# Performance work log

Hardware: AMD Instinct MI355X
Metric: run time of the kernel (lower is better)

Reference implementation:

```python
import jax, jax.numpy as jnp
import numpy as np

D_MODEL = 768
N_HEADS = 4
N_POINTS = 4
PATCH = 16
IMG = 224
HF = IMG // PATCH  # 14
WF = IMG // PATCH  # 14
LQ = HF * WF       # 196 tokens
DH = D_MODEL // N_HEADS  # 192


def setup_inputs() -> dict:
    key = jax.random.key(0)
    ks = jax.random.split(key, 14)
    s = 0.02
    inp = {
        "x": jax.random.normal(ks[0], (4, 16, 3, IMG, IMG), dtype=jnp.float32),
        # patch-embed conv (Conv2d 3->768, k=16, s=16)
        "embed_w": s * jax.random.normal(ks[1], (D_MODEL, 3, PATCH, PATCH), dtype=jnp.float32),
        "embed_b": jnp.zeros((D_MODEL,), dtype=jnp.float32),
        # MSDeformAttn linears (nn.Linear stores W as [out, in]; y = x @ W.T + b)
        "value_w": s * jax.random.normal(ks[2], (D_MODEL, D_MODEL), dtype=jnp.float32),
        "value_b": jnp.zeros((D_MODEL,), dtype=jnp.float32),
        "off_w": s * jax.random.normal(ks[3], (N_HEADS * N_POINTS * 2, D_MODEL), dtype=jnp.float32),
        "off_b": s * jax.random.normal(ks[4], (N_HEADS * N_POINTS * 2,), dtype=jnp.float32),
        "aw_w": s * jax.random.normal(ks[5], (N_HEADS * N_POINTS, D_MODEL), dtype=jnp.float32),
        "aw_b": jnp.zeros((N_HEADS * N_POINTS,), dtype=jnp.float32),
        "outp_w": s * jax.random.normal(ks[6], (D_MODEL, D_MODEL), dtype=jnp.float32),
        "outp_b": jnp.zeros((D_MODEL,), dtype=jnp.float32),
        # final nn.Linear proj
        "proj_w": s * jax.random.normal(ks[7], (D_MODEL, D_MODEL), dtype=jnp.float32),
        "proj_b": jnp.zeros((D_MODEL,), dtype=jnp.float32),
    }
    return inp


def _patch_embed(x, w, b):
    # x: (N,3,H,W); non-overlapping 16x16 patches == Conv2d(3,D,16,16)
    N = x.shape[0]
    xh = x.reshape(N, 3, HF, PATCH, WF, PATCH)
    feat = jnp.einsum('nchpwq,dcpq->nhwd', xh, w) + b  # (N,HF,WF,D)
    return feat.reshape(N, LQ, D_MODEL)


def _ref_points():
    lin = jnp.linspace(0.0, 1.0, HF)
    gy, gx = jnp.meshgrid(lin, lin, indexing='ij')
    return jnp.stack([gx, gy], -1).reshape(LQ, 2)  # (Lq, 2) in [0,1], (x,y)


def _deform_attn_core(value, loc, attn):
    # value: (N, Lq, M, Dh); loc: (N, Lq, M, P, 2) normalized [0,1]; attn: (N, Lq, M, P)
    N = value.shape[0]
    # grid_sample align_corners=False: pixel = (2*loc-1 + 1)*S/2 - 0.5 = loc*S - 0.5
    px = loc[..., 0] * WF - 0.5
    py = loc[..., 1] * HF - 0.5
    x0 = jnp.floor(px).astype(jnp.int32)
    y0 = jnp.floor(py).astype(jnp.int32)
    x1, y1 = x0 + 1, y0 + 1
    wx1 = px - x0.astype(px.dtype)
    wy1 = py - y0.astype(py.dtype)
    wx0, wy0 = 1.0 - wx1, 1.0 - wy1

    valh = value.transpose(0, 2, 1, 3)  # (N, M, HW, Dh)

    def gather(ix, iy):
        valid = (ix >= 0) & (ix < WF) & (iy >= 0) & (iy < HF)  # zeros padding
        idx = jnp.clip(iy, 0, HF - 1) * WF + jnp.clip(ix, 0, WF - 1)
        idxm = idx.transpose(0, 2, 1, 3).reshape(N, N_HEADS, LQ * N_POINTS)
        g = jnp.take_along_axis(valh, idxm[..., None], axis=2)  # (N,M,Lq*P,Dh)
        g = g * valid.transpose(0, 2, 1, 3).reshape(N, N_HEADS, LQ * N_POINTS, 1)
        return g.reshape(N, N_HEADS, LQ, N_POINTS, DH)

    def w4(a, b):  # (N,Lq,M,P) -> (N,M,Lq,P,1)
        return (a * b).transpose(0, 2, 1, 3)[..., None]

    sampled = (w4(wx0, wy0) * gather(x0, y0) + w4(wx1, wy0) * gather(x1, y0)
               + w4(wx0, wy1) * gather(x0, y1) + w4(wx1, wy1) * gather(x1, y1))
    # weighted combine over points
    out = (sampled * attn.transpose(0, 2, 1, 3)[..., None]).sum(3)  # (N,M,Lq,Dh)
    return out.transpose(0, 2, 1, 3).reshape(N, LQ, D_MODEL)


def reference(x, embed_w, embed_b, value_w, value_b, off_w, off_b, aw_w, aw_b,
              outp_w, outp_b, proj_w, proj_b):
    B, T = x.shape[0], x.shape[1]
    N = B * T
    xi = x.reshape(N, 3, IMG, IMG)
    feat = _patch_embed(xi, embed_w, embed_b)  # (N, Lq, D)

    # MSDeformAttn (n_levels=1)
    value = (feat @ value_w.T + value_b).reshape(N, LQ, N_HEADS, DH)
    off = (feat @ off_w.T + off_b).reshape(N, LQ, N_HEADS, N_POINTS, 2)
    aw = (feat @ aw_w.T + aw_b).reshape(N, LQ, N_HEADS, N_POINTS)
    aw = jax.nn.softmax(aw, axis=-1)  # softmax over n_levels*n_points = 4

    ref = _ref_points()  # (Lq, 2)
    norm = jnp.array([WF, HF], dtype=feat.dtype)  # offset_normalizer = (W, H)
    loc = ref[None, :, None, None, :] + off / norm  # (N,Lq,M,P,2)

    out = _deform_attn_core(value, loc, aw)
    out = out @ outp_w.T + outp_b  # output_proj

    pooled = out.mean(axis=1)  # mean over tokens
    final = pooled @ proj_w.T + proj_b
    return final.reshape(B, T, D_MODEL)
```

## Files before the change

### kernel.cpp

```cpp
#include <hip/hip_runtime.h>
#include <hip/hip_bf16.h>


using bf16 = __bf16;
typedef bf16  bf16x4 __attribute__((ext_vector_type(4)));
typedef bf16  bf16x8 __attribute__((ext_vector_type(8)));
typedef float f32x4  __attribute__((ext_vector_type(4)));

#define N_IMG   64
#define LQ      196
#define DM      768
#define NH      4
#define DH      192
#define M_ROWS  (N_IMG * LQ)
#define NCAT    896

#define P_WET    0
#define P_WCAT   288
#define P_BCAT   624
#define P_ZERO   628
#define PREP_GRID 676

#define B_WGEMM   0
#define B_IM2COL  42
#define STAGE_GRID (B_IM2COL + 9408)

#define OFF_A     ((size_t)0)
#define OFF_WC    (OFF_A     + 19267584)
#define OFF_BCAT  (OFF_WC    + 1376256)
#define OFF_VBUF  (OFF_BCAT  + 4096)
#define OFF_OA    (OFF_VBUF  + 19267584)
#define OFF_CORE  (OFF_OA    + 3211264)
#define OFF_POOL  (OFF_CORE  + 196608)
#define OFF_WCATB (OFF_POOL  + 196608)
#define OFF_WET   (OFF_WCATB + 1376256)

__device__ __forceinline__ void gload_lds16(const bf16* g, bf16* l) {
#if __has_builtin(__builtin_amdgcn_global_load_lds)
  __builtin_amdgcn_global_load_lds(
      (const __attribute__((address_space(1))) void*)g,
      (__attribute__((address_space(3))) void*)l, 16, 0, 0);
#else
  *(bf16x8*)l = *(const bf16x8*)g;
#endif
}

__global__ void prep_kernel(const float* __restrict__ embed_w,
                            const float* __restrict__ embed_b,
                            const float* __restrict__ value_w,
                            const float* __restrict__ off_w,
                            const float* __restrict__ aw_w,
                            const float* __restrict__ value_b,
                            const float* __restrict__ off_b,
                            const float* __restrict__ aw_b,
                            bf16* __restrict__ WeT,
                            bf16* __restrict__ Wcatb,
                            float* __restrict__ bcat2,
                            float* __restrict__ core) {
  const int bid = blockIdx.x;
  const int tid = threadIdx.x;

  if (bid < P_WCAT) {
    const int t = bid * 256 + tid;
    const int e = t / 96;
    const int g = t - e * 96;
    bf16x8 o;
#pragma unroll
    for (int j = 0; j < 8; ++j)
      o[j] = (bf16)embed_w[(size_t)(g * 8 + j) * DM + e];
    *(bf16x8*)(WeT + (size_t)e * DM + g * 8) = o;
    return;
  }

  if (bid < P_BCAT) {
    const int t = (bid - P_WCAT) * 256 + tid;
    const int rr = t / 96;
    const int g  = t - rr * 96;
    const float* src = (rr < 768) ? value_w + (size_t)rr * DM
                     : (rr < 800) ? off_w + (size_t)(rr - 768) * DM
                     : (rr < 816) ? aw_w + (size_t)(rr - 800) * DM : nullptr;
    bf16x8 o;
    if (src) {
      const float4 f0 = *(const float4*)(src + g * 8);
      const float4 f1 = *(const float4*)(src + g * 8 + 4);
      o[0] = (bf16)f0.x; o[1] = (bf16)f0.y; o[2] = (bf16)f0.z; o[3] = (bf16)f0.w;
      o[4] = (bf16)f1.x; o[5] = (bf16)f1.y; o[6] = (bf16)f1.z; o[7] = (bf16)f1.w;
    } else {
#pragma unroll
      for (int j = 0; j < 8; ++j) o[j] = (bf16)0.f;
    }
    *(bf16x8*)(Wcatb + (size_t)rr * DM + g * 8) = o;
    return;
  }

  if (bid < P_ZERO) {
    const int o = (bid - P_BCAT) * 256 + tid;
    if (o < NCAT) {
      float bias_o = (o < 768) ? value_b[o]
                   : (o < 800) ? off_b[o - 768]
                   : (o < 816) ? aw_b[o - 800] : 0.f;
      float acc = 0.f;
      if (o < 816) {
        const float* wr = (o < 768) ? value_w + (size_t)o * DM
                        : (o < 800) ? off_w + (size_t)(o - 768) * DM
                        : aw_w + (size_t)(o - 800) * DM;
        const float4* w4p = (const float4*)wr;
        const float4* b4p = (const float4*)embed_b;
#pragma unroll 4
        for (int k = 0; k < DM / 4; ++k) {
          const float4 wv = w4p[k], bv = b4p[k];
          acc += wv.x * bv.x + wv.y * bv.y + wv.z * bv.z + wv.w * bv.w;
        }
      }
      bcat2[o] = acc + bias_o;
    }
    return;
  }

  const int i = (bid - P_ZERO) * 256 + tid;
  f32x4 z = {0.f, 0.f, 0.f, 0.f};
  ((f32x4*)core)[i] = z;
}

__global__ void stage_kernel(const float* __restrict__ x,
                             const bf16* __restrict__ Wcatb,
                             const bf16* __restrict__ WeT,
                             bf16* __restrict__ A,
                             bf16* __restrict__ Wc) {
  const int bid = blockIdx.x;
  const int tid = threadIdx.x;

  if (bid >= B_IM2COL) {
    const int t   = (bid - B_IM2COL) * 256 + tid;
    const int row = t / 192;
    const int j   = t - row * 192;
    const int k   = j * 4;
    const int c   = k >> 8;
    const int r   = k & 255;
    const int p   = r >> 4;
    const int q   = r & 15;
    const int n   = row / 196;
    const int lq  = row - n * 196;
    const int h   = lq / 14;
    const int w   = lq - h * 14;
    const float4 v = *(const float4*)(x +
        ((((size_t)n * 3 + c) * 224) + h * 16 + p) * 224 + w * 16 + q);
    bf16x4 o;
    o[0] = (bf16)v.x; o[1] = (bf16)v.y; o[2] = (bf16)v.z; o[3] = (bf16)v.w;
    *(bf16x4*)(A + (size_t)row * DM + k) = o;
    return;
  }

  const int mT = bid / 6;
  const int nT = bid - mT * 6;
  const int oBase = mT * 128;
  const int eBase = nT * 128;
  const int wave = tid >> 6;
  const int lane = tid & 63;
  const int quad = lane >> 4;
  const int r16  = lane & 15;
  const int wm = wave & 1;
  const int wn = wave >> 1;

  const f32x4 zero = {0.f, 0.f, 0.f, 0.f};
  f32x4 acc[4][4];
#pragma unroll
  for (int mi = 0; mi < 4; ++mi)
#pragma unroll
    for (int ni = 0; ni < 4; ++ni) acc[mi][ni] = zero;

  const bf16* Ab = Wcatb + (size_t)(oBase + wm * 64 + r16) * DM + quad * 8;
  const bf16* Bb = WeT   + (size_t)(eBase + wn * 64 + r16) * DM + quad * 8;

#pragma unroll 2
  for (int kk = 0; kk < DM; kk += 32) {
    bf16x8 af[4], bfr[4];
#pragma unroll
    for (int mi = 0; mi < 4; ++mi)
      af[mi] = *(const bf16x8*)(Ab + (size_t)mi * 16 * DM + kk);
#pragma unroll
    for (int ni = 0; ni < 4; ++ni)
      bfr[ni] = *(const bf16x8*)(Bb + (size_t)ni * 16 * DM + kk);
#pragma unroll
    for (int mi = 0; mi < 4; ++mi)
#pragma unroll
      for (int ni = 0; ni < 4; ++ni)
        acc[mi][ni] = __builtin_amdgcn_mfma_f32_16x16x32_bf16(
            af[mi], bfr[ni], acc[mi][ni], 0, 0, 0);
  }

#pragma unroll
  for (int ni = 0; ni < 4; ++ni) {
    const int col = eBase + wn * 64 + ni * 16 + r16;
#pragma unroll
    for (int mi = 0; mi < 4; ++mi) {
      const int row0 = oBase + wm * 64 + mi * 16 + quad * 4;
#pragma unroll
      for (int rr = 0; rr < 4; ++rr)
        Wc[(size_t)(row0 + rr) * DM + col] = (bf16)acc[mi][ni][rr];
    }
  }
}

__global__ void gemm2_mixed(const bf16* __restrict__ A, const bf16* __restrict__ B,
                            const float* __restrict__ bias,
                            bf16* __restrict__ Vb, float* __restrict__ OA,
                            int M, int N, int K) {
  __shared__ bf16 As[128 * 64];
  __shared__ bf16 Bs[128 * 64];

  const int tid  = threadIdx.x;
  const int wave = tid >> 6;
  const int lane = tid & 63;
  const int nBase = blockIdx.x * 128;
  const int mBase = blockIdx.y * 128;
  const int wm = wave & 1;
  const int wn = wave >> 1;
  const int quad = lane >> 4;
  const int r16  = lane & 15;

  const f32x4 zero = {0.f, 0.f, 0.f, 0.f};
  f32x4 acc[4][4];
#pragma unroll
  for (int mi = 0; mi < 4; ++mi)
#pragma unroll
    for (int ni = 0; ni < 4; ++ni) acc[mi][ni] = zero;

  const int srow = wave * 32 + (lane >> 3);
  const int scol = (lane & 7) * 8;
  const bf16* Ag = A + (size_t)(mBase + srow) * K + scol;
  const bf16* Bg = B + (size_t)(nBase + srow) * K + scol;
  bf16* Al = As + srow * 64 + scol;
  bf16* Bl = Bs + srow * 64 + scol;

  for (int kt = 0; kt < K; kt += 64) {
#pragma unroll
    for (int i = 0; i < 4; ++i) {
      gload_lds16(Ag + (size_t)(i * 8) * K + kt, Al + i * 8 * 64);
      gload_lds16(Bg + (size_t)(i * 8) * K + kt, Bl + i * 8 * 64);
    }
    __syncthreads();
#pragma unroll
    for (int kk = 0; kk < 64; kk += 32) {
      bf16x8 af[4], bfr[4];
#pragma unroll
      for (int mi = 0; mi < 4; ++mi)
        af[mi] = *(const bf16x8*)&As[(wm * 64 + mi * 16 + r16) * 64 + kk + quad * 8];
#pragma unroll
      for (int ni = 0; ni < 4; ++ni)
        bfr[ni] = *(const bf16x8*)&Bs[(wn * 64 + ni * 16 + r16) * 64 + kk + quad * 8];
#pragma unroll
      for (int mi = 0; mi < 4; ++mi)
#pragma unroll
        for (int ni = 0; ni < 4; ++ni)
          acc[mi][ni] = __builtin_amdgcn_mfma_f32_16x16x32_bf16(
              af[mi], bfr[ni], acc[mi][ni], 0, 0, 0);
    }
    __syncthreads();
  }

#pragma unroll
  for (int ni = 0; ni < 4; ++ni) {
    const int col = nBase + wn * 64 + ni * 16 + r16;
    const float bv = bias[col];
#pragma unroll
    for (int mi = 0; mi < 4; ++mi) {
      const int row0 = mBase + wm * 64 + mi * 16 + quad * 4;
#pragma unroll
      for (int rr = 0; rr < 4; ++rr) {
        float v = acc[mi][ni][rr] + bv;
        int row = row0 + rr;
        if (col < 768) {
          Vb[(size_t)row * 768 + col] = (bf16)v;
        } else if (col < 816) {
          OA[(size_t)row * 64 + (col - 768)] = v;
        }
      }
    }
  }
}

__global__ void deform_kernel(const bf16* __restrict__ Vb,
                              const float* __restrict__ OA,
                              float* __restrict__ core) {
  __shared__ float s_w[64][4];
  __shared__ int   s_t[64][4];

  const int n   = blockIdx.x;
  const int lq0 = blockIdx.y * 4;
  const int z   = blockIdx.z;
  const int tid = threadIdx.x;

  if (tid < 64) {
    const int i = tid >> 4;
    const int m = (tid >> 2) & 3;
    const int p = tid & 3;
    const int lq = lq0 + i;
    const float* row = OA + ((size_t)n * LQ + lq) * 64;

    const float l0 = row[32 + m * 4 + 0];
    const float l1 = row[32 + m * 4 + 1];
    const float l2 = row[32 + m * 4 + 2];
    const float l3 = row[32 + m * 4 + 3];
    const float mx = fmaxf(fmaxf(l0, l1), fmaxf(l2, l3));
    const float e0 = __expf(l0 - mx), e1 = __expf(l1 - mx);
    const float e2 = __expf(l2 - mx), e3 = __expf(l3 - mx);
    const float inv = 1.f / (e0 + e1 + e2 + e3);
    const float ep[4] = {e0, e1, e2, e3};
    const float ew = ep[p] * inv;

    const int h = lq / 14, w = lq - (lq / 14) * 14;
    const float px = (float)w * (14.f / 13.f) - 0.5f + row[(m * 4 + p) * 2 + 0];
    const float py = (float)h * (14.f / 13.f) - 0.5f + row[(m * 4 + p) * 2 + 1];
    const float fx = floorf(px), fy = floorf(py);
    const int x0 = (int)fx, y0 = (int)fy;
    const float wx1 = px - fx, wy1 = py - fy;
    const float wx0 = 1.f - wx1, wy0 = 1.f - wy1;

    const bool vx0 = (x0 >= 0) & (x0 < 14);
    const bool vx1 = (x0 >= -1) & (x0 < 13);
    const bool vy0 = (y0 >= 0) & (y0 < 14);
    const bool vy1 = (y0 >= -1) & (y0 < 13);
    const int cx0 = min(max(x0, 0), 13),      cx1 = min(max(x0 + 1, 0), 13);
    const int cy0 = min(max(y0, 0), 13) * 14, cy1 = min(max(y0 + 1, 0), 13) * 14;

    s_w[tid][0] = (vx0 & vy0) ? ew * wx0 * wy0 : 0.f;
    s_w[tid][1] = (vx1 & vy0) ? ew * wx1 * wy0 : 0.f;
    s_w[tid][2] = (vx0 & vy1) ? ew * wx0 * wy1 : 0.f;
    s_w[tid][3] = (vx1 & vy1) ? ew * wx1 * wy1 : 0.f;
    s_t[tid][0] = cy0 + cx0;
    s_t[tid][1] = cy0 + cx1;
    s_t[tid][2] = cy1 + cx0;
    s_t[tid][3] = cy1 + cx1;
  }
  __syncthreads();

  const int ch = z * 256 + tid;
  const int m  = ch / DH;
  const bf16* vb = Vb + (size_t)n * LQ * 768 + ch;
  float acc = 0.f;
#pragma unroll
  for (int i = 0; i < 4; ++i) {
#pragma unroll
    for (int p = 0; p < 4; ++p) {
      const int e = i * 16 + m * 4 + p;
      const float4 w4 = *(const float4*)s_w[e];
      const int4   t4 = *(const int4*)s_t[e];
      acc += w4.x * (float)vb[(size_t)t4.x * 768];
      acc += w4.y * (float)vb[(size_t)t4.y * 768];
      acc += w4.z * (float)vb[(size_t)t4.z * 768];
      acc += w4.w * (float)vb[(size_t)t4.w * 768];
    }
  }
  atomicAdd(&core[(size_t)n * DM + ch], acc * (1.f / 196.f));
}

__global__ void small_linear_ks(const float* __restrict__ in,
                                const float* __restrict__ W,
                                const float* __restrict__ b,
                                float* __restrict__ out) {
  __shared__ float s_in[4 * DM];
  __shared__ float s_red[3][4][64];
  const int tid = threadIdx.x;
  const int n0 = blockIdx.x * 4;
  const float4* src = (const float4*)(in + (size_t)n0 * DM);
#pragma unroll
  for (int i = 0; i < 3; ++i)
    ((float4*)s_in)[tid + i * 256] = src[tid + i * 256];
  __syncthreads();

  const int dl = tid & 63;
  const int ks = tid >> 6;
  const int d  = blockIdx.y * 64 + dl;
  const int k0 = ks * (DM / 4);

  const float4* w4p = (const float4*)(W + (size_t)d * DM + k0);
  const float4* s0 = (const float4*)(s_in + k0);
  const float4* s1 = (const float4*)(s_in + DM + k0);
  const float4* s2 = (const float4*)(s_in + 2 * DM + k0);
  const float4* s3 = (const float4*)(s_in + 3 * DM + k0);
  float a0 = 0.f, a1 = 0.f, a2 = 0.f, a3 = 0.f;
#pragma unroll 8
  for (int k = 0; k < DM / 16; ++k) {
    const float4 w = w4p[k];
    const float4 v0 = s0[k], v1 = s1[k], v2 = s2[k], v3 = s3[k];
    a0 += w.x * v0.x + w.y * v0.y + w.z * v0.z + w.w * v0.w;
    a1 += w.x * v1.x + w.y * v1.y + w.z * v1.z + w.w * v1.w;
    a2 += w.x * v2.x + w.y * v2.y + w.z * v2.z + w.w * v2.w;
    a3 += w.x * v3.x + w.y * v3.y + w.z * v3.z + w.w * v3.w;
  }

  if (ks > 0) {
    s_red[ks - 1][0][dl] = a0;
    s_red[ks - 1][1][dl] = a1;
    s_red[ks - 1][2][dl] = a2;
    s_red[ks - 1][3][dl] = a3;
  }
  __syncthreads();
  if (ks == 0) {
#pragma unroll
    for (int w = 0; w < 3; ++w) {
      a0 += s_red[w][0][dl];
      a1 += s_red[w][1][dl];
      a2 += s_red[w][2][dl];
      a3 += s_red[w][3][dl];
    }
    const float bv = b[d];
    out[(size_t)(n0 + 0) * DM + d] = a0 + bv;
    out[(size_t)(n0 + 1) * DM + d] = a1 + bv;
    out[(size_t)(n0 + 2) * DM + d] = a2 + bv;
    out[(size_t)(n0 + 3) * DM + d] = a3 + bv;
  }
}

extern "C" void kernel_launch(void* const* d_in, const int* in_sizes, int n_in,
                              void* d_out, int out_size, void* d_ws, size_t ws_size,
                              hipStream_t stream) {
  const float* x       = (const float*)d_in[0];
  const float* embed_w = (const float*)d_in[1];
  const float* embed_b = (const float*)d_in[2];
  const float* value_w = (const float*)d_in[3];
  const float* value_b = (const float*)d_in[4];
  const float* off_w   = (const float*)d_in[5];
  const float* off_b   = (const float*)d_in[6];
  const float* aw_w    = (const float*)d_in[7];
  const float* aw_b    = (const float*)d_in[8];
  const float* outp_w  = (const float*)d_in[9];
  const float* outp_b  = (const float*)d_in[10];
  const float* proj_w  = (const float*)d_in[11];
  const float* proj_b  = (const float*)d_in[12];
  float* out = (float*)d_out;

  char* ws = (char*)d_ws;
  bf16*  A      = (bf16*)(ws + OFF_A);
  bf16*  Wc     = (bf16*)(ws + OFF_WC);
  float* bcat2  = (float*)(ws + OFF_BCAT);
  bf16*  Vbuf   = (bf16*)(ws + OFF_VBUF);
  float* OA     = (float*)(ws + OFF_OA);
  float* core   = (float*)(ws + OFF_CORE);
  float* pooled = (float*)(ws + OFF_POOL);
  bf16*  Wcatb  = (bf16*)(ws + OFF_WCATB);
  bf16*  WeT    = (bf16*)(ws + OFF_WET);

  prep_kernel<<<dim3(PREP_GRID), dim3(256), 0, stream>>>(
      embed_w, embed_b, value_w, off_w, aw_w, value_b, off_b, aw_b,
      WeT, Wcatb, bcat2, core);

  stage_kernel<<<dim3(STAGE_GRID), dim3(256), 0, stream>>>(
      x, Wcatb, WeT, A, Wc);

  gemm2_mixed<<<dim3(NCAT / 128, M_ROWS / 128), dim3(256), 0, stream>>>(
      A, Wc, bcat2, Vbuf, OA, M_ROWS, NCAT, DM);

  deform_kernel<<<dim3(N_IMG, 49, 3), dim3(256), 0, stream>>>(Vbuf, OA, core);

  small_linear_ks<<<dim3(N_IMG / 4, DM / 64), dim3(256), 0, stream>>>(
      core, outp_w, outp_b, pooled);
  small_linear_ks<<<dim3(N_IMG / 4, DM / 64), dim3(256), 0, stream>>>(
      pooled, proj_w, proj_b, out);
}
```

Measured before the change: 236.0 us.

## Skip value projection by pooling sampling weights before the linear map

Because the output is mean-pooled over tokens and the value projection is linear, the change collapses each image's bilinear sampling and attention weights into per-head token weights held in shared memory. It applies those weights to the patch features A, then multiplies by the fused value weight once per image. This removes the large 12544x768 value GEMM, the 19 MB bf16 value buffer, and the global atomics. The remaining GEMM computes only the offset and attention columns. The cost is shared-memory atomics, an extra small kernel, and summation in a different order, which slightly changes numerics.

```diff
diff --git a/kernel.cpp b/kernel.cpp
--- a/kernel.cpp
+++ b/kernel.cpp
@@ -18,8 +18,7 @@
 #define P_WET    0
 #define P_WCAT   288
 #define P_BCAT   624
-#define P_ZERO   628
-#define PREP_GRID 676
+#define PREP_GRID 628
 
 #define B_WGEMM   0
 #define B_IM2COL  42
@@ -28,22 +27,13 @@
 #define OFF_A     ((size_t)0)
 #define OFF_WC    (OFF_A     + 19267584)
 #define OFF_BCAT  (OFF_WC    + 1376256)
-#define OFF_VBUF  (OFF_BCAT  + 4096)
-#define OFF_OA    (OFF_VBUF  + 19267584)
+#define OFF_WA    (OFF_BCAT  + 4096)
+#define OFF_SB    (OFF_WA    + 786432)
+#define OFF_OA    (OFF_SB    + 4096)
 #define OFF_CORE  (OFF_OA    + 3211264)
 #define OFF_POOL  (OFF_CORE  + 196608)
 #define OFF_WCATB (OFF_POOL  + 196608)
 #define OFF_WET   (OFF_WCATB + 1376256)
-
-__device__ __forceinline__ void gload_lds16(const bf16* g, bf16* l) {
-#if __has_builtin(__builtin_amdgcn_global_load_lds)
-  __builtin_amdgcn_global_load_lds(
-      (const __attribute__((address_space(1))) void*)g,
-      (__attribute__((address_space(3))) void*)l, 16, 0, 0);
-#else
-  *(bf16x8*)l = *(const bf16x8*)g;
-#endif
-}
 
 __global__ void prep_kernel(const float* __restrict__ embed_w,
                             const float* __restrict__ embed_b,
@@ -55,8 +45,7 @@
                             const float* __restrict__ aw_b,
                             bf16* __restrict__ WeT,
                             bf16* __restrict__ Wcatb,
-                            float* __restrict__ bcat2,
-                            float* __restrict__ core) {
+                            float* __restrict__ bcat2) {
   const int bid = blockIdx.x;
   const int tid = threadIdx.x;
 
@@ -93,33 +82,26 @@
     return;
   }
 
-  if (bid < P_ZERO) {
-    const int o = (bid - P_BCAT) * 256 + tid;
-    if (o < NCAT) {
-      float bias_o = (o < 768) ? value_b[o]
-                   : (o < 800) ? off_b[o - 768]
-                   : (o < 816) ? aw_b[o - 800] : 0.f;
-      float acc = 0.f;
-      if (o < 816) {
-        const float* wr = (o < 768) ? value_w + (size_t)o * DM
-                        : (o < 800) ? off_w + (size_t)(o - 768) * DM
-                        : aw_w + (size_t)(o - 800) * DM;
-        const float4* w4p = (const float4*)wr;
-        const float4* b4p = (const float4*)embed_b;
+  const int o = (bid - P_BCAT) * 256 + tid;
+  if (o < NCAT) {
+    float bias_o = (o < 768) ? value_b[o]
+                 : (o < 800) ? off_b[o - 768]
+                 : (o < 816) ? aw_b[o - 800] : 0.f;
+    float acc = 0.f;
+    if (o < 816) {
+      const float* wr = (o < 768) ? value_w + (size_t)o * DM
+                      : (o < 800) ? off_w + (size_t)(o - 768) * DM
+                      : aw_w + (size_t)(o - 800) * DM;
+      const float4* w4p = (const float4*)wr;
+      const float4* b4p = (const float4*)embed_b;
 #pragma unroll 4
-        for (int k = 0; k < DM / 4; ++k) {
-          const float4 wv = w4p[k], bv = b4p[k];
-          acc += wv.x * bv.x + wv.y * bv.y + wv.z * bv.z + wv.w * bv.w;
-        }
+      for (int k = 0; k < DM / 4; ++k) {
+        const float4 wv = w4p[k], bv = b4p[k];
+        acc += wv.x * bv.x + wv.y * bv.y + wv.z * bv.z + wv.w * bv.w;
       }
-      bcat2[o] = acc + bias_o;
-    }
-    return;
-  }
-
-  const int i = (bid - P_ZERO) * 256 + tid;
-  f32x4 z = {0.f, 0.f, 0.f, 0.f};
-  ((f32x4*)core)[i] = z;
+    }
+    bcat2[o] = acc + bias_o;
+  }
 }
 
 __global__ void stage_kernel(const float* __restrict__ x,
@@ -202,100 +184,62 @@
   }
 }
 
-__global__ void gemm2_mixed(const bf16* __restrict__ A, const bf16* __restrict__ B,
-                            const float* __restrict__ bias,
-                            bf16* __restrict__ Vb, float* __restrict__ OA,
-                            int M, int N, int K) {
-  __shared__ bf16 As[128 * 64];
-  __shared__ bf16 Bs[128 * 64];
-
+__global__ void gemm_oa(const bf16* __restrict__ A, const bf16* __restrict__ Wc,
+                        const float* __restrict__ bcat2, float* __restrict__ OA) {
   const int tid  = threadIdx.x;
   const int wave = tid >> 6;
   const int lane = tid & 63;
-  const int nBase = blockIdx.x * 128;
-  const int mBase = blockIdx.y * 128;
-  const int wm = wave & 1;
-  const int wn = wave >> 1;
   const int quad = lane >> 4;
   const int r16  = lane & 15;
+  const int rBase = blockIdx.x * 64 + wave * 16;
 
   const f32x4 zero = {0.f, 0.f, 0.f, 0.f};
-  f32x4 acc[4][4];
-#pragma unroll
-  for (int mi = 0; mi < 4; ++mi)
-#pragma unroll
-    for (int ni = 0; ni < 4; ++ni) acc[mi][ni] = zero;
-
-  const int srow = wave * 32 + (lane >> 3);
-  const int scol = (lane & 7) * 8;
-  const bf16* Ag = A + (size_t)(mBase + srow) * K + scol;
-  const bf16* Bg = B + (size_t)(nBase + srow) * K + scol;
-  bf16* Al = As + srow * 64 + scol;
-  bf16* Bl = Bs + srow * 64 + scol;
-
-  for (int kt = 0; kt < K; kt += 64) {
-#pragma unroll
-    for (int i = 0; i < 4; ++i) {
-      gload_lds16(Ag + (size_t)(i * 8) * K + kt, Al + i * 8 * 64);
-      gload_lds16(Bg + (size_t)(i * 8) * K + kt, Bl + i * 8 * 64);
-    }
-    __syncthreads();
-#pragma unroll
-    for (int kk = 0; kk < 64; kk += 32) {
-      bf16x8 af[4], bfr[4];
-#pragma unroll
-      for (int mi = 0; mi < 4; ++mi)
-        af[mi] = *(const bf16x8*)&As[(wm * 64 + mi * 16 + r16) * 64 + kk + quad * 8];
-#pragma unroll
-      for (int ni = 0; ni < 4; ++ni)
-        bfr[ni] = *(const bf16x8*)&Bs[(wn * 64 + ni * 16 + r16) * 64 + kk + quad * 8];
-#pragma unroll
-      for (int mi = 0; mi < 4; ++mi)
-#pragma unroll
-        for (int ni = 0; ni < 4; ++ni)
-          acc[mi][ni] = __builtin_amdgcn_mfma_f32_16x16x32_bf16(
-              af[mi], bfr[ni], acc[mi][ni], 0, 0, 0);
-    }
-    __syncthreads();
-  }
-
-#pragma unroll
-  for (int ni = 0; ni < 4; ++ni) {
-    const int col = nBase + wn * 64 + ni * 16 + r16;
-    const float bv = bias[col];
-#pragma unroll
-    for (int mi = 0; mi < 4; ++mi) {
-      const int row0 = mBase + wm * 64 + mi * 16 + quad * 4;
-#pragma unroll
-      for (int rr = 0; rr < 4; ++rr) {
-        float v = acc[mi][ni][rr] + bv;
-        int row = row0 + rr;
-        if (col < 768) {
-          Vb[(size_t)row * 768 + col] = (bf16)v;
-        } else if (col < 816) {
-          OA[(size_t)row * 64 + (col - 768)] = v;
-        }
-      }
-    }
-  }
-}
-
-__global__ void deform_kernel(const bf16* __restrict__ Vb,
-                              const float* __restrict__ OA,
-                              float* __restrict__ core) {
-  __shared__ float s_w[64][4];
-  __shared__ int   s_t[64][4];
-
+  f32x4 acc[3];
+#pragma unroll
+  for (int ni = 0; ni < 3; ++ni) acc[ni] = zero;
+
+  const bf16* Ab = A  + (size_t)(rBase + r16) * DM + quad * 8;
+  const bf16* Bb = Wc + (size_t)(768 + r16) * DM + quad * 8;
+
+#pragma unroll 4
+  for (int kk = 0; kk < DM; kk += 32) {
+    bf16x8 af = *(const bf16x8*)(Ab + kk);
+    bf16x8 b0 = *(const bf16x8*)(Bb + kk);
+    bf16x8 b1 = *(const bf16x8*)(Bb + (size_t)16 * DM + kk);
+    bf16x8 b2 = *(const bf16x8*)(Bb + (size_t)32 * DM + kk);
+    acc[0] = __builtin_amdgcn_mfma_f32_16x16x32_bf16(af, b0, acc[0], 0, 0, 0);
+    acc[1] = __builtin_amdgcn_mfma_f32_16x16x32_bf16(af, b1, acc[1], 0, 0, 0);
+    acc[2] = __builtin_amdgcn_mfma_f32_16x16x32_bf16(af, b2, acc[2], 0, 0, 0);
+  }
+
+#pragma unroll
+  for (int ni = 0; ni < 3; ++ni) {
+    const int o = ni * 16 + r16;
+    const float bv = bcat2[768 + o];
+#pragma unroll
+    for (int rr = 0; rr < 4; ++rr) {
+      const int row = rBase + quad * 4 + rr;
+      OA[(size_t)row * 64 + o] = acc[ni][rr] + bv;
+    }
+  }
+}
+
+__global__ void deform_wa(const bf16* __restrict__ A,
+                          const float* __restrict__ OA,
+                          float* __restrict__ wa,
+                          float* __restrict__ sb) {
+  __shared__ float s_ws[4][196];
   const int n   = blockIdx.x;
-  const int lq0 = blockIdx.y * 4;
-  const int z   = blockIdx.z;
+  const int yq  = blockIdx.y;
   const int tid = threadIdx.x;
 
-  if (tid < 64) {
-    const int i = tid >> 4;
-    const int m = (tid >> 2) & 3;
-    const int p = tid & 3;
-    const int lq = lq0 + i;
+  for (int i = tid; i < 4 * 196; i += 192) ((float*)s_ws)[i] = 0.f;
+  __syncthreads();
+
+  for (int it = tid; it < 3136; it += 192) {
+    const int lq = it >> 4;
+    const int m  = (it >> 2) & 3;
+    const int p  = it & 3;
     const float* row = OA + ((size_t)n * LQ + lq) * 64;
 
     const float l0 = row[32 + m * 4 + 0];
@@ -324,35 +268,109 @@
     const int cx0 = min(max(x0, 0), 13),      cx1 = min(max(x0 + 1, 0), 13);
     const int cy0 = min(max(y0, 0), 13) * 14, cy1 = min(max(y0 + 1, 0), 13) * 14;
 
-    s_w[tid][0] = (vx0 & vy0) ? ew * wx0 * wy0 : 0.f;
-    s_w[tid][1] = (vx1 & vy0) ? ew * wx1 * wy0 : 0.f;
-    s_w[tid][2] = (vx0 & vy1) ? ew * wx0 * wy1 : 0.f;
-    s_w[tid][3] = (vx1 & vy1) ? ew * wx1 * wy1 : 0.f;
-    s_t[tid][0] = cy0 + cx0;
-    s_t[tid][1] = cy0 + cx1;
-    s_t[tid][2] = cy1 + cx0;
-    s_t[tid][3] = cy1 + cx1;
-  }
-  __syncthreads();
-
-  const int ch = z * 256 + tid;
-  const int m  = ch / DH;
-  const bf16* vb = Vb + (size_t)n * LQ * 768 + ch;
-  float acc = 0.f;
-#pragma unroll
-  for (int i = 0; i < 4; ++i) {
-#pragma unroll
-    for (int p = 0; p < 4; ++p) {
-      const int e = i * 16 + m * 4 + p;
-      const float4 w4 = *(const float4*)s_w[e];
-      const int4   t4 = *(const int4*)s_t[e];
-      acc += w4.x * (float)vb[(size_t)t4.x * 768];
-      acc += w4.y * (float)vb[(size_t)t4.y * 768];
-      acc += w4.z * (float)vb[(size_t)t4.z * 768];
-      acc += w4.w * (float)vb[(size_t)t4.w * 768];
-    }
-  }
-  atomicAdd(&core[(size_t)n * DM + ch], acc * (1.f / 196.f));
+    const float w0 = (vx0 & vy0) ? ew * wx0 * wy0 : 0.f;
+    const float w1 = (vx1 & vy0) ? ew * wx1 * wy0 : 0.f;
+    const float w2 = (vx0 & vy1) ? ew * wx0 * wy1 : 0.f;
+    const float w3 = (vx1 & vy1) ? ew * wx1 * wy1 : 0.f;
+    atomicAdd(&s_ws[m][cy0 + cx0], w0);
+    atomicAdd(&s_ws[m][cy0 + cx1], w1);
+    atomicAdd(&s_ws[m][cy1 + cx0], w2);
+    atomicAdd(&s_ws[m][cy1 + cx1], w3);
+  }
+  __syncthreads();
+
+  const int k = yq * 192 + tid;
+  const bf16* ap = A + (size_t)n * LQ * DM + k;
+  float wam0 = 0.f, wam1 = 0.f, wam2 = 0.f, wam3 = 0.f;
+#pragma unroll 4
+  for (int tok = 0; tok < 196; ++tok) {
+    const float a = (float)ap[(size_t)tok * DM];
+    wam0 += s_ws[0][tok] * a;
+    wam1 += s_ws[1][tok] * a;
+    wam2 += s_ws[2][tok] * a;
+    wam3 += s_ws[3][tok] * a;
+  }
+  float* wp = wa + (size_t)n * 4 * DM + k;
+  wp[0 * DM] = wam0;
+  wp[1 * DM] = wam1;
+  wp[2 * DM] = wam2;
+  wp[3 * DM] = wam3;
+
+  if (yq == 0 && tid < 4) {
+    float s = 0.f;
+    for (int tok = 0; tok < 196; ++tok) s += s_ws[tid][tok];
+    sb[n * 4 + tid] = s;
+  }
+}
+
+__global__ void core_wsum(const float* __restrict__ wa,
+                          const float* __restrict__ sb,
+                          const bf16* __restrict__ Wc,
+                          const float* __restrict__ bcat2,
+                          float* __restrict__ core) {
+  __shared__ float s_wa[4 * DM];
+  __shared__ float s_red[3][4][64];
+  __shared__ float s_sbv[4];
+  const int tid = threadIdx.x;
+  const int n0  = blockIdx.x * 4;
+  const int m   = blockIdx.y / 3;
+
+#pragma unroll
+  for (int i = 0; i < 3; ++i) {
+    const int t   = tid + i * 256;
+    const int img = t / 192;
+    const int k4  = t - img * 192;
+    ((float4*)s_wa)[(size_t)img * 192 + k4] =
+        ((const float4*)(wa + ((size_t)(n0 + img) * 4 + m) * DM))[k4];
+  }
+  if (tid < 4) s_sbv[tid] = sb[(n0 + tid) * 4 + m];
+  __syncthreads();
+
+  const int dl = tid & 63;
+  const int ks = tid >> 6;
+  const int d  = blockIdx.y * 64 + dl;
+  const int k0 = ks * 192;
+
+  const bf16* wrow = Wc + (size_t)d * DM + k0;
+  const float* p0 = s_wa + 0 * DM + k0;
+  const float* p1 = s_wa + 1 * DM + k0;
+  const float* p2 = s_wa + 2 * DM + k0;
+  const float* p3 = s_wa + 3 * DM + k0;
+  float a0 = 0.f, a1 = 0.f, a2 = 0.f, a3 = 0.f;
+#pragma unroll 4
+  for (int k = 0; k < 192; k += 8) {
+    const bf16x8 wv = *(const bf16x8*)(wrow + k);
+#pragma unroll
+    for (int j = 0; j < 8; ++j) {
+      const float w = (float)wv[j];
+      a0 += w * p0[k + j];
+      a1 += w * p1[k + j];
+      a2 += w * p2[k + j];
+      a3 += w * p3[k + j];
+    }
+  }
+
+  if (ks > 0) {
+    s_red[ks - 1][0][dl] = a0;
+    s_red[ks - 1][1][dl] = a1;
+    s_red[ks - 1][2][dl] = a2;
+    s_red[ks - 1][3][dl] = a3;
+  }
+  __syncthreads();
+  if (ks == 0) {
+#pragma unroll
+    for (int w = 0; w < 3; ++w) {
+      a0 += s_red[w][0][dl];
+      a1 += s_red[w][1][dl];
+      a2 += s_red[w][2][dl];
+      a3 += s_red[w][3][dl];
+    }
+    const float bv = bcat2[d];
+    core[(size_t)(n0 + 0) * DM + d] = (a0 + s_sbv[0] * bv) * (1.f / 196.f);
+    core[(size_t)(n0 + 1) * DM + d] = (a1 + s_sbv[1] * bv) * (1.f / 196.f);
+    core[(size_t)(n0 + 2) * DM + d] = (a2 + s_sbv[2] * bv) * (1.f / 196.f);
+    core[(size_t)(n0 + 3) * DM + d] = (a3 + s_sbv[3] * bv) * (1.f / 196.f);
+  }
 }
 
 __global__ void small_linear_ks(const float* __restrict__ in,
@@ -435,7 +453,8 @@
   bf16*  A      = (bf16*)(ws + OFF_A);
   bf16*  Wc     = (bf16*)(ws + OFF_WC);
   float* bcat2  = (float*)(ws + OFF_BCAT);
-  bf16*  Vbuf   = (bf16*)(ws + OFF_VBUF);
+  float* wa     = (float*)(ws + OFF_WA);
+  float* sb     = (float*)(ws + OFF_SB);
   float* OA     = (float*)(ws + OFF_OA);
   float* core   = (float*)(ws + OFF_CORE);
   float* pooled = (float*)(ws + OFF_POOL);
@@ -444,15 +463,17 @@
 
   prep_kernel<<<dim3(PREP_GRID), dim3(256), 0, stream>>>(
       embed_w, embed_b, value_w, off_w, aw_w, value_b, off_b, aw_b,
-      WeT, Wcatb, bcat2, core);
+      WeT, Wcatb, bcat2);
 
   stage_kernel<<<dim3(STAGE_GRID), dim3(256), 0, stream>>>(
       x, Wcatb, WeT, A, Wc);
 
-  gemm2_mixed<<<dim3(NCAT / 128, M_ROWS / 128), dim3(256), 0, stream>>>(
-      A, Wc, bcat2, Vbuf, OA, M_ROWS, NCAT, DM);
-
-  deform_kernel<<<dim3(N_IMG, 49, 3), dim3(256), 0, stream>>>(Vbuf, OA, core);
+  gemm_oa<<<dim3(M_ROWS / 64), dim3(256), 0, stream>>>(A, Wc, bcat2, OA);
+
+  deform_wa<<<dim3(N_IMG, 4), dim3(192), 0, stream>>>(A, OA, wa, sb);
+
+  core_wsum<<<dim3(N_IMG / 4, DM / 64), dim3(256), 0, stream>>>(
+      wa, sb, Wc, bcat2, core);
 
   small_linear_ks<<<dim3(N_IMG / 4, DM / 64), dim3(256), 0, stream>>>(
       core, outp_w, outp_b, pooled);
```

New measurement: 241.1 us. 2.2% more time.
